# Kernel tuning notes

Hardware: AMD Instinct MI355X
Metric: run time of the kernel (lower is better)

Reference implementation:

```python
import jax, jax.numpy as jnp
import numpy as np

H, W, C_IN, C_OUT, N = 512, 512, 256, 256, 65536


def setup_inputs() -> dict:
    key = jax.random.key(0)
    k1, k2, k3, k4 = jax.random.split(key, 4)
    feature = jax.random.normal(k1, (1, C_IN, H, W), dtype=jnp.float32)
    weight = jax.random.normal(k2, (C_OUT, C_IN, 3, 3), dtype=jnp.float32) * 0.05
    # base sparse locations in the unpadded map; build 3x3 neighborhood indices
    # into the PADDED ([H+2, W+2]) map, exactly like F.pad + fancy indexing.
    base_h = jax.random.randint(k3, (N,), 0, H, dtype=jnp.int32)
    base_w = jax.random.randint(k4, (N,), 0, W, dtype=jnp.int32)
    dh = jnp.repeat(jnp.arange(3, dtype=jnp.int32), 3)  # [9]: 0,0,0,1,1,1,2,2,2
    dw = jnp.tile(jnp.arange(3, dtype=jnp.int32), 3)    # [9]: 0,1,2,0,1,2,...
    h_idx = base_h[None, :] + dh[:, None]  # [9, N], values in [0, H+1]
    w_idx = base_w[None, :] + dw[:, None]  # [9, N], values in [0, W+1]
    return {"feature": feature, "weight": weight, "h_idx": h_idx, "w_idx": w_idx}


def reference(feature, weight, h_idx, w_idx):
    # feature: [1, C, H, W]; weight: [Cout, C, 3, 3]; h_idx/w_idx: [9, N]
    C = feature.shape[1]
    out_ch = weight.shape[0]
    # F.pad(feature, [1,1,1,1])[0] -> [C, H+2, W+2]
    padded = jnp.pad(feature, ((0, 0), (0, 0), (1, 1), (1, 1)))[0]
    # gather 3x3 neighborhoods at sparse locations -> [C, 9, N]
    gathered = padded[:, h_idx, w_idx]
    # .view(9*C, -1): contiguous reshape gives row index c*9 + k
    g = gathered.reshape(C * 9, -1)  # [C*9, N]
    # kernel_d2s = weight.view(out, -1): row ordering c*9 + (kh*3+kw) matches
    k2d = weight.reshape(out_ch, -1)  # [Cout, C*9]
    return k2d @ g  # [Cout, N]
```

## Files before the change

### kernel.cpp

```cpp
#include <hip/hip_runtime.h>
#include <hip/hip_bf16.h>

#define HH 512
#define WW 512
#define CIN 256
#define COUT 256
#define NPTS 65536
#define PW 514
#define NPIX (PW * PW)
#define NKT 72

typedef __bf16 bf16x8 __attribute__((ext_vector_type(8)));
typedef float f32x16 __attribute__((ext_vector_type(16)));
typedef unsigned short us8 __attribute__((ext_vector_type(8)));

static __device__ __forceinline__ unsigned short f2bf(float f) {
  unsigned u = __builtin_bit_cast(unsigned, f);
  unsigned r = u + 0x7fffu + ((u >> 16) & 1u);
  return (unsigned short)(r >> 16);
}

static __device__ __forceinline__ void gload16(const void* g, void* l) {
  __builtin_amdgcn_global_load_lds(
      (const __attribute__((address_space(1))) unsigned int*)g,
      (__attribute__((address_space(3))) unsigned int*)l, 16, 0, 0);
}

__global__ __launch_bounds__(256) void prep_weight(const float* __restrict__ w,
                                                   unsigned short* __restrict__ A) {
  int i = blockIdx.x * 256 + threadIdx.x;
  int kt = i >> 13;
  int o  = i & 8191;
  int r  = o >> 5;
  int cp = (o >> 3) & 3;
  int j  = o & 7;
  int c  = cp ^ ((r >> 1) & 3);
  int k  = kt * 32 + c * 8 + j;
  int t  = k >> 8;
  int ci = k & 255;
  A[i] = f2bf(__builtin_nontemporal_load(&w[r * 2304 + ci * 9 + t]));
}

__global__ __launch_bounds__(256) void border_zero(unsigned short* __restrict__ Ft) {
  int g = blockIdx.x * 256 + threadIdx.x;
  if (g >= 2052 * 32) return;
  int p = g >> 5, c = g & 31;
  int py, px;
  if (p < 514)        { py = 0;        px = p; }
  else if (p < 1028)  { py = 513;      px = p - 514; }
  else if (p < 1540)  { py = p - 1027; px = 0; }
  else                { py = p - 1539; px = 513; }
  *(us8*)&Ft[((size_t)py * PW + px) * 256 + c * 8] = (us8){0, 0, 0, 0, 0, 0, 0, 0};
}

__global__ __launch_bounds__(256) void transpose_feat(const float* __restrict__ f,
                                                      unsigned short* __restrict__ Ft) {
  __shared__ unsigned short lds[64 * 264];
  int pix0 = blockIdx.x * 64;
  int y = pix0 >> 9, x0 = pix0 & 511;
  int tid = threadIdx.x;
  int p = tid & 63;
  int cb = tid >> 6;
  const float* src = f + pix0 + p;
  for (int c8 = 0; c8 < 8; ++c8) {
    us8 v;
#pragma unroll
    for (int j = 0; j < 8; ++j) {
      int ci = cb * 64 + c8 * 8 + j;
      v[j] = f2bf(__builtin_nontemporal_load(&src[ci * 262144]));
    }
    *(us8*)&lds[p * 264 + cb * 64 + c8 * 8] = v;
  }
  __syncthreads();
  int cic = tid & 31;
  int pr = tid >> 5;
  for (int g = 0; g < 8; ++g) {
    int p2 = pr + g * 8;
    us8 v = *(const us8*)&lds[p2 * 264 + cic * 8];
    *(us8*)&Ft[((size_t)((y + 1) * PW + x0 + 1 + p2)) * 256 + cic * 8] = v;
  }
}

__global__ __launch_bounds__(512, 2) void gemm_gather(
    const unsigned short* __restrict__ A,
    const unsigned short* __restrict__ Ft,
    const int* __restrict__ hidx,
    const int* __restrict__ widx,
    float* __restrict__ out) {
  __shared__ unsigned short lds[73728];
  unsigned short* ldsB = lds + 24576;

  int tid = threadIdx.x;
  int lane = tid & 63, wv = tid >> 6;
  int wm = wv & 1, wn = wv >> 1;
  int n0 = blockIdx.x << 8;

  int pxc = tid >> 3;
  int lcB = (tid & 7) ^ (pxc & 7);
  const unsigned short *FtP0, *FtP1, *FtP2, *FtP3;
  {
    FtP0 = Ft + (long)(hidx[n0 + pxc] * PW + widx[n0 + pxc]) * 256 + lcB * 8;
    FtP1 = Ft + (long)(hidx[n0 + 64 + pxc] * PW + widx[n0 + 64 + pxc]) * 256 + lcB * 8;
    FtP2 = Ft + (long)(hidx[n0 + 128 + pxc] * PW + widx[n0 + 128 + pxc]) * 256 + lcB * 8;
    FtP3 = Ft + (long)(hidx[n0 + 192 + pxc] * PW + widx[n0 + 192 + pxc]) * 256 + lcB * 8;
  }

#define STAGE_A(t_, ab_)                                                      \
  do {                                                                        \
    const unsigned short* g_ = A + (size_t)(t_) * 8192 + tid * 8;             \
    unsigned short* l_ = lds + (ab_) * 8192 + tid * 8;                        \
    gload16(g_, l_);                                                          \
    gload16(g_ + 4096, l_ + 4096);                                            \
  } while (0)

#define STAGE_BP(q_, bb_)                                                     \
  do {                                                                        \
    int tap_ = (q_) >> 2;                                                     \
    long off_ = (long)((tap_ / 3) * PW + (tap_ - (tap_ / 3) * 3)) * 256 +     \
                ((q_) & 3) * 64;                                              \
    unsigned short* l_ = ldsB + (bb_) * 16384 + tid * 8;                      \
    gload16(FtP0 + off_, l_);                                                 \
    gload16(FtP1 + off_, l_ + 4096);                                         \
    gload16(FtP2 + off_, l_ + 8192);                                          \
    gload16(FtP3 + off_, l_ + 12288);                                         \
  } while (0)

#define LDA(dst, ab_, kg_, mt_)                                               \
  do {                                                                        \
    int r_ = wm * 128 + (mt_) * 32 + (lane & 31);                             \
    int c_ = ((kg_) * 2 + (lane >> 5)) ^ ((r_ >> 1) & 3);                     \
    dst = *(const bf16x8*)&lds[(ab_) * 8192 + r_ * 32 + c_ * 8];              \
  } while (0)

#define LDB(dst, bb_, s_, kg_, nt_)                                           \
  do {                                                                        \
    int col_ = wn * 64 + (nt_) * 32 + (lane & 31);                            \
    int ph_ = ((s_) * 4 + (kg_) * 2 + (lane >> 5)) ^ (col_ & 7);              \
    dst = *(const bf16x8*)&ldsB[(bb_) * 16384 + col_ * 64 + ph_ * 8];         \
  } while (0)

#define MF(x_, y_, z_) __builtin_amdgcn_mfma_f32_32x32x16_bf16(x_, y_, z_, 0, 0, 0)

#define SYNC_LGKM()                                                           \
  do {                                                                        \
    __builtin_amdgcn_s_barrier();                                             \
    asm volatile("s_waitcnt lgkmcnt(0)" ::: "memory");                        \
    __builtin_amdgcn_sched_barrier(0);                                        \
  } while (0)

#define TILE(ab_, bb_, s_, STGA, STGB)                                        \
  do {                                                                        \
    bf16x8 a0, a1, a2, a3, b0, b1, b2, b3;                                    \
    LDA(a0, ab_, 0, 0); LDA(a1, ab_, 0, 1);                                   \
    LDA(a2, ab_, 1, 0); LDA(a3, ab_, 1, 1);                                   \
    LDB(b0, bb_, s_, 0, 0); LDB(b1, bb_, s_, 0, 1);                           \
    LDB(b2, bb_, s_, 1, 0); LDB(b3, bb_, s_, 1, 1);                           \
    STGA;                                                                     \
    SYNC_LGKM();                                                              \
    __builtin_amdgcn_s_setprio(1);                                            \
    acc[0][0] = MF(a0, b0, acc[0][0]); acc[0][1] = MF(a0, b1, acc[0][1]);     \
    acc[1][0] = MF(a1, b0, acc[1][0]); acc[1][1] = MF(a1, b1, acc[1][1]);     \
    acc[0][0] = MF(a2, b2, acc[0][0]); acc[0][1] = MF(a2, b3, acc[0][1]);     \
    acc[1][0] = MF(a3, b2, acc[1][0]); acc[1][1] = MF(a3, b3, acc[1][1]);     \
    __builtin_amdgcn_s_setprio(0);                                            \
    __builtin_amdgcn_s_barrier();                                             \
    LDA(a0, ab_, 0, 2); LDA(a1, ab_, 0, 3);                                   \
    LDA(a2, ab_, 1, 2); LDA(a3, ab_, 1, 3);                                   \
    STGB;                                                                     \
    SYNC_LGKM();                                                              \
    __builtin_amdgcn_s_setprio(1);                                            \
    acc[2][0] = MF(a0, b0, acc[2][0]); acc[2][1] = MF(a0, b1, acc[2][1]);     \
    acc[3][0] = MF(a1, b0, acc[3][0]); acc[3][1] = MF(a1, b1, acc[3][1]);     \
    acc[2][0] = MF(a2, b2, acc[2][0]); acc[2][1] = MF(a2, b3, acc[2][1]);     \
    acc[3][0] = MF(a3, b2, acc[3][0]); acc[3][1] = MF(a3, b3, acc[3][1]);     \
    __builtin_amdgcn_s_setprio(0);                                            \
    asm volatile("s_waitcnt vmcnt(6)" ::: "memory");                          \
    __builtin_amdgcn_s_barrier();                                             \
  } while (0)

  f32x16 acc[4][2];
#pragma unroll
  for (int mt = 0; mt < 4; ++mt)
#pragma unroll
    for (int nt = 0; nt < 2; ++nt)
      acc[mt][nt] = (f32x16)(0.f);

  STAGE_BP(0, 0);
  STAGE_A(0, 0);
  STAGE_A(1, 1);
  STAGE_BP(1, 1);
  asm volatile("s_waitcnt vmcnt(6)" ::: "memory");
  __builtin_amdgcn_s_barrier();

  for (int P3 = 0; P3 < 12; ++P3) {
#pragma unroll
    for (int v = 0; v < 3; ++v) {
      int q = P3 * 3 + v;
      int t = 2 * q;
      TILE((2 * v) % 3, v, 0,
           STAGE_A((t + 2 < NKT ? t + 2 : NKT - 1), (2 * v + 2) % 3),
           STAGE_BP((q + 2 < 36 ? q + 2 : 35), (v + 2) % 3));
      TILE((2 * v + 1) % 3, v, 1,
           STAGE_A((t + 3 < NKT ? t + 3 : NKT - 1), (2 * v) % 3),
           (void)0);
    }
  }

#undef STAGE_A
#undef STAGE_BP
#undef LDA
#undef LDB
#undef MF
#undef SYNC_LGKM
#undef TILE

  int colb = n0 + wn * 64 + (lane & 31);
  int rb = wm * 128 + ((lane >> 5) << 2);
#pragma unroll
  for (int mt = 0; mt < 4; ++mt)
#pragma unroll
    for (int nt = 0; nt < 2; ++nt)
#pragma unroll
      for (int r = 0; r < 16; ++r) {
        int row = rb + mt * 32 + (r & 3) + ((r >> 2) << 3);
        __builtin_nontemporal_store(acc[mt][nt][r],
                                    &out[(size_t)row * NPTS + colb + nt * 32]);
      }
}

__global__ __launch_bounds__(256) void naive_conv(const float* __restrict__ f,
                                                  const float* __restrict__ w,
                                                  const int* __restrict__ hi,
                                                  const int* __restrict__ wi,
                                                  float* __restrict__ out) {
  int idx = blockIdx.x * 256 + threadIdx.x;
  int n = idx & (NPTS - 1);
  int co = idx >> 16;
  int bh = hi[n] - 1;
  int bw = wi[n] - 1;
  float acc = 0.f;
  for (int ci = 0; ci < CIN; ++ci) {
    const float* fc = f + (size_t)ci * 262144;
    const float* wc = w + (size_t)co * 2304 + ci * 9;
#pragma unroll
    for (int t = 0; t < 9; ++t) {
      int y = bh + t / 3, x = bw + t % 3;
      float v = (y >= 0 && y < 512 && x >= 0 && x < 512) ? fc[y * 512 + x] : 0.f;
      acc += wc[t] * v;
    }
  }
  out[(size_t)co * NPTS + n] = acc;
}

extern "C" void kernel_launch(void* const* d_in, const int* in_sizes, int n_in,
                              void* d_out, int out_size, void* d_ws, size_t ws_size,
                              hipStream_t stream) {
  const float* feature = (const float*)d_in[0];
  const float* weight  = (const float*)d_in[1];
  const int* hidx      = (const int*)d_in[2];
  const int* widx      = (const int*)d_in[3];
  float* out           = (float*)d_out;

  const size_t FT_OFF = 2ull * 1024 * 1024;
  const size_t FT_BYTES = (size_t)NPIX * 256 * 2;
  const size_t NEED = FT_OFF + FT_BYTES;

  if (ws_size >= NEED) {
    unsigned short* Abf = (unsigned short*)d_ws;
    unsigned short* Ft = (unsigned short*)((char*)d_ws + FT_OFF);
    prep_weight<<<(NKT * 8192) / 256, 256, 0, stream>>>(weight, Abf);
    border_zero<<<(2052 * 32 + 255) / 256, 256, 0, stream>>>(Ft);
    transpose_feat<<<262144 / 64, 256, 0, stream>>>(feature, Ft);
    gemm_gather<<<NPTS / 256, 512, 0, stream>>>(Abf, Ft, hidx, widx, out);
  } else {
    naive_conv<<<(COUT * NPTS) / 256, 256, 0, stream>>>(feature, weight, hidx, widx, out);
  }
}
```

Baseline: 161.2 us.

## Halve gemm N-tile to 128 and raise occupancy with single-phase pipeline

Shrinks each gemm block's point tile from 256 to 128 columns, with warps arranged 4x2 over M and N. The per-warp accumulator drops from 4x2 to 2x2 MFMA tiles, and LDS use drops from 144KB to 80KB per block. Launch bounds move from 2 to 4 waves per SIMD so more blocks can be resident. The A pipeline goes from triple to double buffering, and each tile now has a single wait-and-barrier head instead of two sync points. In exchange, the weight tiles are re-read from global twice as often per output, and the shallower A prefetch may expose load latency.

```diff
diff --git a/kernel.cpp b/kernel.cpp
--- a/kernel.cpp
+++ b/kernel.cpp
@@ -81,28 +81,26 @@
   }
 }
 
-__global__ __launch_bounds__(512, 2) void gemm_gather(
+__global__ __launch_bounds__(512, 4) void gemm_gather(
     const unsigned short* __restrict__ A,
     const unsigned short* __restrict__ Ft,
     const int* __restrict__ hidx,
     const int* __restrict__ widx,
     float* __restrict__ out) {
-  __shared__ unsigned short lds[73728];
-  unsigned short* ldsB = lds + 24576;
+  __shared__ unsigned short lds[40960];
+  unsigned short* ldsB = lds + 16384;
 
   int tid = threadIdx.x;
   int lane = tid & 63, wv = tid >> 6;
-  int wm = wv & 1, wn = wv >> 1;
-  int n0 = blockIdx.x << 8;
-
-  int pxc = tid >> 3;
-  int lcB = (tid & 7) ^ (pxc & 7);
-  const unsigned short *FtP0, *FtP1, *FtP2, *FtP3;
+  int wm = wv & 3, wn = wv >> 2;
+  int n0 = blockIdx.x << 7;
+
+  int cq = tid >> 3;
+  int lcB = (tid & 7) ^ (cq & 7);
+  const unsigned short *FtP0, *FtP1;
   {
-    FtP0 = Ft + (long)(hidx[n0 + pxc] * PW + widx[n0 + pxc]) * 256 + lcB * 8;
-    FtP1 = Ft + (long)(hidx[n0 + 64 + pxc] * PW + widx[n0 + 64 + pxc]) * 256 + lcB * 8;
-    FtP2 = Ft + (long)(hidx[n0 + 128 + pxc] * PW + widx[n0 + 128 + pxc]) * 256 + lcB * 8;
-    FtP3 = Ft + (long)(hidx[n0 + 192 + pxc] * PW + widx[n0 + 192 + pxc]) * 256 + lcB * 8;
+    FtP0 = Ft + (long)(hidx[n0 + cq] * PW + widx[n0 + cq]) * 256 + lcB * 8;
+    FtP1 = Ft + (long)(hidx[n0 + 64 + cq] * PW + widx[n0 + 64 + cq]) * 256 + lcB * 8;
   }
 
 #define STAGE_A(t_, ab_)                                                      \
@@ -118,16 +116,14 @@
     int tap_ = (q_) >> 2;                                                     \
     long off_ = (long)((tap_ / 3) * PW + (tap_ - (tap_ / 3) * 3)) * 256 +     \
                 ((q_) & 3) * 64;                                              \
-    unsigned short* l_ = ldsB + (bb_) * 16384 + tid * 8;                      \
+    unsigned short* l_ = ldsB + (bb_) * 8192 + tid * 8;                       \
     gload16(FtP0 + off_, l_);                                                 \
-    gload16(FtP1 + off_, l_ + 4096);                                         \
-    gload16(FtP2 + off_, l_ + 8192);                                          \
-    gload16(FtP3 + off_, l_ + 12288);                                         \
+    gload16(FtP1 + off_, l_ + 4096);                                          \
   } while (0)
 
 #define LDA(dst, ab_, kg_, mt_)                                               \
   do {                                                                        \
-    int r_ = wm * 128 + (mt_) * 32 + (lane & 31);                             \
+    int r_ = wm * 64 + (mt_) * 32 + (lane & 31);                              \
     int c_ = ((kg_) * 2 + (lane >> 5)) ^ ((r_ >> 1) & 3);                     \
     dst = *(const bf16x8*)&lds[(ab_) * 8192 + r_ * 32 + c_ * 8];              \
   } while (0)
@@ -136,73 +132,57 @@
   do {                                                                        \
     int col_ = wn * 64 + (nt_) * 32 + (lane & 31);                            \
     int ph_ = ((s_) * 4 + (kg_) * 2 + (lane >> 5)) ^ (col_ & 7);              \
-    dst = *(const bf16x8*)&ldsB[(bb_) * 16384 + col_ * 64 + ph_ * 8];         \
+    dst = *(const bf16x8*)&ldsB[(bb_) * 8192 + col_ * 64 + ph_ * 8];          \
   } while (0)
 
 #define MF(x_, y_, z_) __builtin_amdgcn_mfma_f32_32x32x16_bf16(x_, y_, z_, 0, 0, 0)
 
-#define SYNC_LGKM()                                                           \
-  do {                                                                        \
+#define HEAD(W_)                                                              \
+  do {                                                                        \
+    asm volatile("s_waitcnt lgkmcnt(0)" ::: "memory");                        \
+    asm volatile("s_waitcnt vmcnt(" #W_ ")" ::: "memory");                    \
     __builtin_amdgcn_s_barrier();                                             \
-    asm volatile("s_waitcnt lgkmcnt(0)" ::: "memory");                        \
     __builtin_amdgcn_sched_barrier(0);                                        \
   } while (0)
 
-#define TILE(ab_, bb_, s_, STGA, STGB)                                        \
-  do {                                                                        \
-    bf16x8 a0, a1, a2, a3, b0, b1, b2, b3;                                    \
+#define TILE(ab_, bb_, s_, W_, ...)                                           \
+  do {                                                                        \
+    HEAD(W_);                                                                 \
+    bf16x8 a0, a1, b0, b1, a2, a3, b2, b3;                                    \
     LDA(a0, ab_, 0, 0); LDA(a1, ab_, 0, 1);                                   \
+    LDB(b0, bb_, s_, 0, 0); LDB(b1, bb_, s_, 0, 1);                           \
+    __VA_ARGS__;                                                              \
     LDA(a2, ab_, 1, 0); LDA(a3, ab_, 1, 1);                                   \
-    LDB(b0, bb_, s_, 0, 0); LDB(b1, bb_, s_, 0, 1);                           \
     LDB(b2, bb_, s_, 1, 0); LDB(b3, bb_, s_, 1, 1);                           \
-    STGA;                                                                     \
-    SYNC_LGKM();                                                              \
     __builtin_amdgcn_s_setprio(1);                                            \
     acc[0][0] = MF(a0, b0, acc[0][0]); acc[0][1] = MF(a0, b1, acc[0][1]);     \
     acc[1][0] = MF(a1, b0, acc[1][0]); acc[1][1] = MF(a1, b1, acc[1][1]);     \
     acc[0][0] = MF(a2, b2, acc[0][0]); acc[0][1] = MF(a2, b3, acc[0][1]);     \
     acc[1][0] = MF(a3, b2, acc[1][0]); acc[1][1] = MF(a3, b3, acc[1][1]);     \
     __builtin_amdgcn_s_setprio(0);                                            \
-    __builtin_amdgcn_s_barrier();                                             \
-    LDA(a0, ab_, 0, 2); LDA(a1, ab_, 0, 3);                                   \
-    LDA(a2, ab_, 1, 2); LDA(a3, ab_, 1, 3);                                   \
-    STGB;                                                                     \
-    SYNC_LGKM();                                                              \
-    __builtin_amdgcn_s_setprio(1);                                            \
-    acc[2][0] = MF(a0, b0, acc[2][0]); acc[2][1] = MF(a0, b1, acc[2][1]);     \
-    acc[3][0] = MF(a1, b0, acc[3][0]); acc[3][1] = MF(a1, b1, acc[3][1]);     \
-    acc[2][0] = MF(a2, b2, acc[2][0]); acc[2][1] = MF(a2, b3, acc[2][1]);     \
-    acc[3][0] = MF(a3, b2, acc[3][0]); acc[3][1] = MF(a3, b3, acc[3][1]);     \
-    __builtin_amdgcn_s_setprio(0);                                            \
-    asm volatile("s_waitcnt vmcnt(6)" ::: "memory");                          \
-    __builtin_amdgcn_s_barrier();                                             \
-  } while (0)
-
-  f32x16 acc[4][2];
-#pragma unroll
-  for (int mt = 0; mt < 4; ++mt)
+  } while (0)
+
+  f32x16 acc[2][2];
+#pragma unroll
+  for (int mt = 0; mt < 2; ++mt)
 #pragma unroll
     for (int nt = 0; nt < 2; ++nt)
       acc[mt][nt] = (f32x16)(0.f);
 
+  STAGE_A(0, 0);
   STAGE_BP(0, 0);
-  STAGE_A(0, 0);
-  STAGE_A(1, 1);
   STAGE_BP(1, 1);
-  asm volatile("s_waitcnt vmcnt(6)" ::: "memory");
-  __builtin_amdgcn_s_barrier();
 
   for (int P3 = 0; P3 < 12; ++P3) {
 #pragma unroll
     for (int v = 0; v < 3; ++v) {
       int q = P3 * 3 + v;
       int t = 2 * q;
-      TILE((2 * v) % 3, v, 0,
-           STAGE_A((t + 2 < NKT ? t + 2 : NKT - 1), (2 * v + 2) % 3),
+      TILE(0, v, 0, 0,
+           STAGE_A(t + 1, 1);
            STAGE_BP((q + 2 < 36 ? q + 2 : 35), (v + 2) % 3));
-      TILE((2 * v + 1) % 3, v, 1,
-           STAGE_A((t + 3 < NKT ? t + 3 : NKT - 1), (2 * v) % 3),
-           (void)0);
+      TILE(1, v, 1, 2,
+           STAGE_A((t + 2 < NKT ? t + 2 : NKT - 1), 0));
     }
   }
 
@@ -211,13 +191,13 @@
 #undef LDA
 #undef LDB
 #undef MF
-#undef SYNC_LGKM
+#undef HEAD
 #undef TILE
 
   int colb = n0 + wn * 64 + (lane & 31);
-  int rb = wm * 128 + ((lane >> 5) << 2);
-#pragma unroll
-  for (int mt = 0; mt < 4; ++mt)
+  int rb = wm * 64 + ((lane >> 5) << 2);
+#pragma unroll
+  for (int mt = 0; mt < 2; ++mt)
 #pragma unroll
     for (int nt = 0; nt < 2; ++nt)
 #pragma unroll
@@ -271,7 +251,7 @@
     prep_weight<<<(NKT * 8192) / 256, 256, 0, stream>>>(weight, Abf);
     border_zero<<<(2052 * 32 + 255) / 256, 256, 0, stream>>>(Ft);
     transpose_feat<<<262144 / 64, 256, 0, stream>>>(feature, Ft);
-    gemm_gather<<<NPTS / 256, 512, 0, stream>>>(Abf, Ft, hidx, widx, out);
+    gemm_gather<<<NPTS / 128, 512, 0, stream>>>(Abf, Ft, hidx, widx, out);
   } else {
     naive_conv<<<(COUT * NPTS) / 256, 256, 0, stream>>>(feature, weight, hidx, widx, out);
   }
```

Result: no change. 163.2 us (+1.3%).
